# Kernel optimization log

Hardware: AMD Instinct MI355X
Metric: run time of the kernel (lower is better)

Reference implementation:

```python
import jax, jax.numpy as jnp
import numpy as np

N, D, G, H, M = 500000, 128, 64, 128, 256  # bag size, local_dim, global_dim, attn_hidden, mlp_hidden
TEMP = 1.0


def setup_inputs() -> dict:
    key = jax.random.key(0)
    ks = jax.random.split(key, 8)
    s = 0.05
    return {
        "bag": jax.random.normal(ks[0], (N, D), jnp.float32),
        "global_feat": jax.random.normal(ks[1], (G,), jnp.float32),
        # attention_V: Linear(D, H) + Tanh
        "Wv": jax.random.normal(ks[2], (H, D), jnp.float32) * s,
        "bv": jnp.zeros((H,), jnp.float32),
        # attention_U: Linear(D, H) + Sigmoid
        "Wu": jax.random.normal(ks[3], (H, D), jnp.float32) * s,
        "bu": jnp.zeros((H,), jnp.float32),
        # attention_weights: Linear(H, 1)
        "Ww": jax.random.normal(ks[4], (1, H), jnp.float32) * s,
        "bw": jnp.zeros((1,), jnp.float32),
        "W1": jax.random.normal(ks[5], (M, D + G), jnp.float32) * s,
        "b1": jnp.zeros((M,), jnp.float32),
        "W2": jax.random.normal(ks[6], (1, M), jnp.float32) * s,
        "b2": jnp.zeros((1,), jnp.float32),
    }


def reference(bag, global_feat, Wv, bv, Wu, bu, Ww, bw, W1, b1, W2, b2):
    # feature_extractor = Identity (use_feature_extractor=False); dropout = identity (eval)
    V = jnp.tanh(bag @ Wv.T + bv)            # [N, H]
    U = jax.nn.sigmoid(bag @ Wu.T + bu)      # [N, H]
    Ggate = V * U                            # [N, H]
    A_raw = Ggate @ Ww.T + bw                # [N, 1]
    alpha = jax.nn.softmax(A_raw / TEMP, axis=0)  # softmax over bag dim
    bag_embedding = alpha.T @ bag            # [1, D]
    fused = jnp.concatenate([bag_embedding, global_feat.reshape(1, -1)], axis=1)  # [1, D+G]
    h = jax.nn.leaky_relu(fused @ W1.T + b1, negative_slope=0.01)  # [1, M]
    score = h @ W2.T + b2                    # [1, 1]
    return (score, alpha)
```

## Files before the change

### kernel.cpp

```cpp
#include <hip/hip_runtime.h>
#include <hip/hip_bf16.h>

#define N_BAG 500000
#define DIM   128
#define ROWS_PER_ITER 32
#define ITERS 21
#define ROWS_PER_BLOCK 672
#define NBLK  768
#define GDIM  64
#define LDB   136

typedef __attribute__((ext_vector_type(8))) __bf16 bf16x8;
typedef __attribute__((ext_vector_type(4))) __bf16 bf16x4;
typedef __attribute__((ext_vector_type(4))) float  f32x4;

union BF8 { bf16x8 v; __bf16 e[8]; };

__device__ __forceinline__ float fast_rcp(float x) { return __builtin_amdgcn_rcpf(x); }

__global__ __launch_bounds__(256, 3)
void attn_pass1(const float* __restrict__ bag,
                const float* __restrict__ Wv, const float* __restrict__ bv,
                const float* __restrict__ Wu, const float* __restrict__ bu,
                const float* __restrict__ Ww, const float* __restrict__ bw,
                float* __restrict__ aOut,
                float* __restrict__ blkS, float* __restrict__ blkW,
                float* __restrict__ Eacc, float* __restrict__ Ssum)
{
    __shared__ __align__(16) unsigned char smem[2 * ROWS_PER_ITER * LDB * 2];
    __shared__ __align__(16) float a_part[ROWS_PER_ITER][4];

    typedef __bf16 XsRow[ROWS_PER_ITER][LDB];
    XsRow* Xs = (XsRow*)smem;
    float (*fin)[4] = (float(*)[4])smem;

    const int tid = threadIdx.x;
    const int w   = tid >> 6;
    const int L   = tid & 63;
    const int m16 = L & 15;
    const int q   = L >> 4;
    const int hh  = L >> 5;
    const int c32 = L & 31;
    const int blk = blockIdx.x;
    const int rowBase = blk * ROWS_PER_BLOCK;

    if (blk == 0) {
        if (tid < DIM) Eacc[tid] = 0.0f;
        if (tid == DIM) Ssum[0] = 0.0f;
    }

    BF8 fv[2][4], fu[2][4];
    float bvv[2], buu[2], www[2];
#pragma unroll
    for (int ht = 0; ht < 2; ++ht) {
        const int h = w*32 + ht*16 + m16;
        bvv[ht] = bv[h]; buu[ht] = bu[h]; www[ht] = Ww[h];
#pragma unroll
        for (int s = 0; s < 4; ++s) {
            const int d0 = s*32 + q*8;
            const float4 v0 = *(const float4*)(Wv + h*DIM + d0);
            const float4 v1 = *(const float4*)(Wv + h*DIM + d0 + 4);
            const float4 u0 = *(const float4*)(Wu + h*DIM + d0);
            const float4 u1 = *(const float4*)(Wu + h*DIM + d0 + 4);
            fv[ht][s].e[0]=(__bf16)v0.x; fv[ht][s].e[1]=(__bf16)v0.y;
            fv[ht][s].e[2]=(__bf16)v0.z; fv[ht][s].e[3]=(__bf16)v0.w;
            fv[ht][s].e[4]=(__bf16)v1.x; fv[ht][s].e[5]=(__bf16)v1.y;
            fv[ht][s].e[6]=(__bf16)v1.z; fv[ht][s].e[7]=(__bf16)v1.w;
            fu[ht][s].e[0]=(__bf16)u0.x; fu[ht][s].e[1]=(__bf16)u0.y;
            fu[ht][s].e[2]=(__bf16)u0.z; fu[ht][s].e[3]=(__bf16)u0.w;
            fu[ht][s].e[4]=(__bf16)u1.x; fu[ht][s].e[5]=(__bf16)u1.y;
            fu[ht][s].e[6]=(__bf16)u1.z; fu[ht][s].e[7]=(__bf16)u1.w;
        }
    }
    const float bw0 = bw[0];

    float4 stg[4];
#pragma unroll
    for (int i = 0; i < 4; ++i) {
        int r = rowBase + i*8 + w*2 + hh;
        if (r >= N_BAG) r = N_BAG - 1;
        stg[i] = *(const float4*)(bag + (size_t)r*DIM + c32*4);
    }

    float s_acc = 0.0f;
    float wacc0 = 0.f, wacc1 = 0.f, wacc2 = 0.f, wacc3 = 0.f;

    for (int it = 0; it < ITERS; ++it) {
        const int buf = it & 1;
        const int tileStart = rowBase + it*ROWS_PER_ITER;

#pragma unroll
        for (int i = 0; i < 4; ++i) {
            const int row = i*8 + w*2 + hh;
            bf16x4 pk;
            pk.x = (__bf16)stg[i].x; pk.y = (__bf16)stg[i].y;
            pk.z = (__bf16)stg[i].z; pk.w = (__bf16)stg[i].w;
            *(bf16x4*)&Xs[buf][row][c32*4] = pk;
        }
        __syncthreads();

        if (it + 1 < ITERS) {
            const int ts2 = tileStart + ROWS_PER_ITER;
#pragma unroll
            for (int i = 0; i < 4; ++i) {
                int r = ts2 + i*8 + w*2 + hh;
                if (r >= N_BAG) r = N_BAG - 1;
                stg[i] = *(const float4*)(bag + (size_t)r*DIM + c32*4);
            }
        }

#pragma unroll
        for (int r = 0; r < 2; ++r) {
            f32x4 accV[2], accU[2];
#pragma unroll
            for (int ht = 0; ht < 2; ++ht) {
                accV[ht] = (f32x4){0.f,0.f,0.f,0.f};
                accU[ht] = (f32x4){0.f,0.f,0.f,0.f};
            }
#pragma unroll
            for (int s = 0; s < 4; ++s) {
                const bf16x8 af = *(const bf16x8*)&Xs[buf][r*16 + m16][s*32 + q*8];
#pragma unroll
                for (int ht = 0; ht < 2; ++ht) {
                    accV[ht] = __builtin_amdgcn_mfma_f32_16x16x32_bf16(af, fv[ht][s].v, accV[ht], 0, 0, 0);
                    accU[ht] = __builtin_amdgcn_mfma_f32_16x16x32_bf16(af, fu[ht][s].v, accU[ht], 0, 0, 0);
                }
            }
            float psum[4];
#pragma unroll
            for (int g = 0; g < 4; ++g) {
                float p = 0.0f;
#pragma unroll
                for (int ht = 0; ht < 2; ++ht) {
                    const float z = accV[ht][g] + bvv[ht];
                    const float y = accU[ht][g] + buu[ht];
                    const float A = __expf(2.0f*z);
                    const float B = __expf(y);
                    p += (A - 1.0f) * B * www[ht] * fast_rcp((A + 1.0f) * (B + 1.0f));
                }
                p += __shfl_xor(p, 1); p += __shfl_xor(p, 2);
                p += __shfl_xor(p, 4); p += __shfl_xor(p, 8);
                psum[g] = p;
            }
            if (m16 == 0) {
#pragma unroll
                for (int g = 0; g < 4; ++g)
                    a_part[r*16 + q*4 + g][w] = psum[g];
            }
        }
        __syncthreads();

        const int li = L & 31;
        const float4 ap = *(const float4*)&a_part[li][0];
        float a = ap.x + ap.y + ap.z + ap.w + bw0;
        const int grow = tileStart + li;
        if (w == 0 && L < 32 && grow < N_BAG) aOut[grow] = a;
        if (grow >= N_BAG) a = -1e30f;
        const float e = __expf(a);
        if (w == 0 && L < 32) s_acc += e;

        float s0 = 0.f, s1 = 0.f, s2 = 0.f, s3 = 0.f;
#pragma unroll
        for (int i = 0; i < 4; ++i) {
            const int row = i*8 + w*2 + hh;
            const float ei = __shfl(e, row);
            const bf16x4 xb = *(const bf16x4*)&Xs[buf][row][c32*4];
            s0 += ei * (float)xb.x; s1 += ei * (float)xb.y;
            s2 += ei * (float)xb.z; s3 += ei * (float)xb.w;
        }
        wacc0 += s0; wacc1 += s1; wacc2 += s2; wacc3 += s3;
    }

    float st = s_acc;
    st += __shfl_xor(st, 1);  st += __shfl_xor(st, 2);
    st += __shfl_xor(st, 4);  st += __shfl_xor(st, 8);
    st += __shfl_xor(st, 16); st += __shfl_xor(st, 32);

    __syncthreads();
    fin[tid][0] = wacc0; fin[tid][1] = wacc1;
    fin[tid][2] = wacc2; fin[tid][3] = wacc3;
    if (L == 0) a_part[0][w] = st;
    __syncthreads();
    if (tid < 128) {
        float v = 0.0f;
#pragma unroll
        for (int k = 0; k < 8; ++k) {
            const int t = (k >> 1)*64 + (k & 1)*32 + (tid >> 2);
            v += fin[t][tid & 3];
        }
        blkW[blk*DIM + tid] = v;
    }
    if (tid == 0) blkS[blk] = a_part[0][0];

    (void)Eacc; (void)Ssum;
}

__global__ void headA(const float* __restrict__ blkW, const float* __restrict__ blkS,
                      float* __restrict__ E, float* __restrict__ Ssum)
{
    const int tid = threadIdx.x;
    const int c = tid & 127, g = tid >> 7;
    const int b0 = blockIdx.x * 16;
    float acc = 0.0f;
#pragma unroll
    for (int t = 0; t < 8; ++t) {
        const int b = b0 + g*8 + t;
        acc += blkW[b*DIM + c];
    }
    atomicAdd(&E[c], acc);

    if (tid < 16) {
        float sv = blkS[b0 + tid];
        sv += __shfl_xor(sv, 1); sv += __shfl_xor(sv, 2);
        sv += __shfl_xor(sv, 4); sv += __shfl_xor(sv, 8);
        if (tid == 0) atomicAdd(Ssum, sv);
    }
}

__global__ void headB(const float* __restrict__ E, const float* __restrict__ Ssum,
                      const float* __restrict__ gfeat,
                      const float* __restrict__ W1, const float* __restrict__ b1,
                      const float* __restrict__ W2, const float* __restrict__ b2,
                      float* __restrict__ out)
{
    __shared__ float f[DIM + GDIM];
    __shared__ float red[256];
    const int tid = threadIdx.x;

    const float invS = 1.0f / Ssum[0];
    if (tid < DIM)             f[tid] = E[tid] * invS;
    else if (tid < DIM + GDIM) f[tid] = gfeat[tid - DIM];
    __syncthreads();

    float a2 = b1[tid];
    const float4* w1p = (const float4*)(W1 + tid * (DIM + GDIM));
    const float4* fp  = (const float4*)f;
#pragma unroll 4
    for (int k = 0; k < (DIM + GDIM) / 4; ++k) {
        const float4 a4 = w1p[k]; const float4 f4 = fp[k];
        a2 += a4.x*f4.x + a4.y*f4.y + a4.z*f4.z + a4.w*f4.w;
    }
    const float h = a2 > 0.0f ? a2 : 0.01f * a2;
    red[tid] = h * W2[tid]; __syncthreads();
    for (int s = 128; s > 0; s >>= 1) {
        if (tid < s) red[tid] += red[tid + s];
        __syncthreads();
    }
    if (tid == 0) out[0] = red[0] + b2[0];
}

__global__ void alpha_kernel(float* __restrict__ alpha, const float* __restrict__ Ssum)
{
    const int i = blockIdx.x * blockDim.x + threadIdx.x;
    const float invS = 1.0f / Ssum[0];
    if (i * 4 < N_BAG) {
        float4 a4 = *(float4*)(alpha + i*4);
        a4.x = __expf(a4.x) * invS; a4.y = __expf(a4.y) * invS;
        a4.z = __expf(a4.z) * invS; a4.w = __expf(a4.w) * invS;
        *(float4*)(alpha + i*4) = a4;
    }
}

extern "C" void kernel_launch(void* const* d_in, const int* in_sizes, int n_in,
                              void* d_out, int out_size, void* d_ws, size_t ws_size,
                              hipStream_t stream)
{
    const float* bag   = (const float*)d_in[0];
    const float* gfeat = (const float*)d_in[1];
    const float* Wv    = (const float*)d_in[2];
    const float* bv    = (const float*)d_in[3];
    const float* Wu    = (const float*)d_in[4];
    const float* bu    = (const float*)d_in[5];
    const float* Ww    = (const float*)d_in[6];
    const float* bw    = (const float*)d_in[7];
    const float* W1    = (const float*)d_in[8];
    const float* b1    = (const float*)d_in[9];
    const float* W2    = (const float*)d_in[10];
    const float* b2    = (const float*)d_in[11];
    float* out = (float*)d_out;
    float* ws  = (float*)d_ws;

    float* blkS = ws;
    float* blkW = ws + 1024;
    float* Eacc = ws + 1024 + 98304;
    float* Ssum = ws + 1024 + 98304 + 128;

    attn_pass1<<<NBLK, 256, 0, stream>>>(bag, Wv, bv, Wu, bu, Ww, bw,
                                         out + 1, blkS, blkW, Eacc, Ssum);
    headA<<<48, 256, 0, stream>>>(blkW, blkS, Eacc, Ssum);
    headB<<<1, 256, 0, stream>>>(Eacc, Ssum, gfeat, W1, b1, W2, b2, out);
    alpha_kernel<<<(N_BAG/4 + 255) / 256, 256, 0, stream>>>(out + 1, Ssum);
}
```

Before: 399.8 us.

## Register double-buffer bag tiles, single LDS buffer, fuse head into alpha kernel

The attention pass now keeps two register staging sets and alternates between them in an unrolled pair loop, so only one LDS tile buffer is needed. The softmax-weighted accumulation reads the fp32 staged registers instead of re-reading bf16 values from LDS, and the biases are folded into the MFMA accumulator initialization. The single-block MLP head is merged into the alpha-normalization kernel, removing one kernel launch. The aim is to cut LDS traffic and launch overhead, at the cost of higher register pressure from holding two staging sets.

```diff
diff --git a/kernel.cpp b/kernel.cpp
--- a/kernel.cpp
+++ b/kernel.cpp
@@ -27,11 +27,11 @@
                 float* __restrict__ blkS, float* __restrict__ blkW,
                 float* __restrict__ Eacc, float* __restrict__ Ssum)
 {
-    __shared__ __align__(16) unsigned char smem[2 * ROWS_PER_ITER * LDB * 2];
+    __shared__ __align__(16) unsigned char smem[ROWS_PER_ITER * LDB * 2];
     __shared__ __align__(16) float a_part[ROWS_PER_ITER][4];
 
-    typedef __bf16 XsRow[ROWS_PER_ITER][LDB];
-    XsRow* Xs = (XsRow*)smem;
+    typedef __bf16 XsT[LDB];
+    XsT* Xs = (XsT*)smem;
     float (*fin)[4] = (float(*)[4])smem;
 
     const int tid = threadIdx.x;
@@ -74,102 +74,98 @@
     }
     const float bw0 = bw[0];
 
-    float4 stg[4];
-#pragma unroll
-    for (int i = 0; i < 4; ++i) {
-        int r = rowBase + i*8 + w*2 + hh;
-        if (r >= N_BAG) r = N_BAG - 1;
-        stg[i] = *(const float4*)(bag + (size_t)r*DIM + c32*4);
-    }
-
     float s_acc = 0.0f;
     float wacc0 = 0.f, wacc1 = 0.f, wacc2 = 0.f, wacc3 = 0.f;
-
-    for (int it = 0; it < ITERS; ++it) {
-        const int buf = it & 1;
-        const int tileStart = rowBase + it*ROWS_PER_ITER;
-
-#pragma unroll
-        for (int i = 0; i < 4; ++i) {
-            const int row = i*8 + w*2 + hh;
-            bf16x4 pk;
-            pk.x = (__bf16)stg[i].x; pk.y = (__bf16)stg[i].y;
-            pk.z = (__bf16)stg[i].z; pk.w = (__bf16)stg[i].w;
-            *(bf16x4*)&Xs[buf][row][c32*4] = pk;
-        }
-        __syncthreads();
-
-        if (it + 1 < ITERS) {
-            const int ts2 = tileStart + ROWS_PER_ITER;
-#pragma unroll
-            for (int i = 0; i < 4; ++i) {
-                int r = ts2 + i*8 + w*2 + hh;
-                if (r >= N_BAG) r = N_BAG - 1;
-                stg[i] = *(const float4*)(bag + (size_t)r*DIM + c32*4);
-            }
-        }
-
-#pragma unroll
-        for (int r = 0; r < 2; ++r) {
-            f32x4 accV[2], accU[2];
-#pragma unroll
-            for (int ht = 0; ht < 2; ++ht) {
-                accV[ht] = (f32x4){0.f,0.f,0.f,0.f};
-                accU[ht] = (f32x4){0.f,0.f,0.f,0.f};
-            }
-#pragma unroll
-            for (int s = 0; s < 4; ++s) {
-                const bf16x8 af = *(const bf16x8*)&Xs[buf][r*16 + m16][s*32 + q*8];
-#pragma unroll
-                for (int ht = 0; ht < 2; ++ht) {
-                    accV[ht] = __builtin_amdgcn_mfma_f32_16x16x32_bf16(af, fv[ht][s].v, accV[ht], 0, 0, 0);
-                    accU[ht] = __builtin_amdgcn_mfma_f32_16x16x32_bf16(af, fu[ht][s].v, accU[ht], 0, 0, 0);
-                }
-            }
-            float psum[4];
-#pragma unroll
-            for (int g = 0; g < 4; ++g) {
-                float p = 0.0f;
-#pragma unroll
-                for (int ht = 0; ht < 2; ++ht) {
-                    const float z = accV[ht][g] + bvv[ht];
-                    const float y = accU[ht][g] + buu[ht];
-                    const float A = __expf(2.0f*z);
-                    const float B = __expf(y);
-                    p += (A - 1.0f) * B * www[ht] * fast_rcp((A + 1.0f) * (B + 1.0f));
-                }
-                p += __shfl_xor(p, 1); p += __shfl_xor(p, 2);
-                p += __shfl_xor(p, 4); p += __shfl_xor(p, 8);
-                psum[g] = p;
-            }
-            if (m16 == 0) {
-#pragma unroll
-                for (int g = 0; g < 4; ++g)
-                    a_part[r*16 + q*4 + g][w] = psum[g];
-            }
-        }
-        __syncthreads();
-
-        const int li = L & 31;
-        const float4 ap = *(const float4*)&a_part[li][0];
-        float a = ap.x + ap.y + ap.z + ap.w + bw0;
-        const int grow = tileStart + li;
-        if (w == 0 && L < 32 && grow < N_BAG) aOut[grow] = a;
-        if (grow >= N_BAG) a = -1e30f;
-        const float e = __expf(a);
-        if (w == 0 && L < 32) s_acc += e;
-
-        float s0 = 0.f, s1 = 0.f, s2 = 0.f, s3 = 0.f;
-#pragma unroll
-        for (int i = 0; i < 4; ++i) {
-            const int row = i*8 + w*2 + hh;
-            const float ei = __shfl(e, row);
-            const bf16x4 xb = *(const bf16x4*)&Xs[buf][row][c32*4];
-            s0 += ei * (float)xb.x; s1 += ei * (float)xb.y;
-            s2 += ei * (float)xb.z; s3 += ei * (float)xb.w;
-        }
-        wacc0 += s0; wacc1 += s1; wacc2 += s2; wacc3 += s3;
-    }
+    float4 stgA[4], stgB[4];
+
+#define LOADT(DST, T) do {                                                    \
+    const int ts_ = rowBase + (T)*ROWS_PER_ITER;                              \
+    _Pragma("unroll")                                                         \
+    for (int i_ = 0; i_ < 4; ++i_) {                                          \
+        int r_ = ts_ + i_*8 + w*2 + hh;                                       \
+        if (r_ >= N_BAG) r_ = N_BAG - 1;                                      \
+        DST[i_] = *(const float4*)(bag + (size_t)r_*DIM + c32*4);             \
+    } } while (0)
+
+#define STEP(T, CUR, NXT, DO_PF) do {                                         \
+    _Pragma("unroll")                                                         \
+    for (int i_ = 0; i_ < 4; ++i_) {                                          \
+        const int row_ = i_*8 + w*2 + hh;                                     \
+        bf16x4 pk_;                                                           \
+        pk_.x = (__bf16)CUR[i_].x; pk_.y = (__bf16)CUR[i_].y;                 \
+        pk_.z = (__bf16)CUR[i_].z; pk_.w = (__bf16)CUR[i_].w;                 \
+        *(bf16x4*)&Xs[row_][c32*4] = pk_;                                     \
+    }                                                                         \
+    __syncthreads();                 \
+    if (DO_PF) LOADT(NXT, (T) + 1);                                           \
+    _Pragma("unroll")                                                         \
+    for (int r_ = 0; r_ < 2; ++r_) {                                          \
+        f32x4 accV_[2], accU_[2];                                             \
+        _Pragma("unroll")                                                     \
+        for (int ht_ = 0; ht_ < 2; ++ht_) {                                   \
+            accV_[ht_] = (f32x4){bvv[ht_], bvv[ht_], bvv[ht_], bvv[ht_]};     \
+            accU_[ht_] = (f32x4){buu[ht_], buu[ht_], buu[ht_], buu[ht_]};     \
+        }                                                                     \
+        _Pragma("unroll")                                                     \
+        for (int s_ = 0; s_ < 4; ++s_) {                                      \
+            const bf16x8 af_ = *(const bf16x8*)&Xs[r_*16 + m16][s_*32 + q*8]; \
+            _Pragma("unroll")                                                 \
+            for (int ht_ = 0; ht_ < 2; ++ht_) {                               \
+                accV_[ht_] = __builtin_amdgcn_mfma_f32_16x16x32_bf16(af_, fv[ht_][s_].v, accV_[ht_], 0, 0, 0); \
+                accU_[ht_] = __builtin_amdgcn_mfma_f32_16x16x32_bf16(af_, fu[ht_][s_].v, accU_[ht_], 0, 0, 0); \
+            }                                                                 \
+        }                                                                     \
+        \
+        float psum_[4];                                                       \
+        _Pragma("unroll")                                                     \
+        for (int g_ = 0; g_ < 4; ++g_) {                                      \
+            float p_ = 0.0f;                                                  \
+            _Pragma("unroll")                                                 \
+            for (int ht_ = 0; ht_ < 2; ++ht_) {                               \
+                const float z_ = accV_[ht_][g_];       \
+                const float y_ = accU_[ht_][g_];                              \
+                const float A_ = __expf(2.0f*z_);                             \
+                const float B_ = __expf(y_);                                  \
+                p_ += (A_ - 1.0f) * B_ * www[ht_] * fast_rcp((A_ + 1.0f) * (B_ + 1.0f)); \
+            }                                                                 \
+            p_ += __shfl_xor(p_, 1); p_ += __shfl_xor(p_, 2);                 \
+            p_ += __shfl_xor(p_, 4); p_ += __shfl_xor(p_, 8);                 \
+            psum_[g_] = p_;                                                   \
+        }                                                                     \
+        if (m16 == 0) {                                                       \
+            _Pragma("unroll")                                                 \
+            for (int g_ = 0; g_ < 4; ++g_)                                    \
+                a_part[r_*16 + q*4 + g_][w] = psum_[g_];                      \
+        }                                                                     \
+    }                                                                         \
+    __syncthreads();              \
+    {                                                                         \
+        const int li_ = L & 31;                                               \
+        const float4 ap_ = *(const float4*)&a_part[li_][0];                   \
+        float a_ = ap_.x + ap_.y + ap_.z + ap_.w + bw0;                       \
+        const int grow_ = rowBase + (T)*ROWS_PER_ITER + li_;                  \
+        if (w == 0 && L < 32 && grow_ < N_BAG) aOut[grow_] = a_;              \
+        if (grow_ >= N_BAG) a_ = -1e30f;    \
+        const float e_ = __expf(a_);                                          \
+        if (w == 0 && L < 32) s_acc += e_;         \
+        _Pragma("unroll")                                                     \
+        for (int i_ = 0; i_ < 4; ++i_) {                                      \
+            const int row_ = i_*8 + w*2 + hh;                                 \
+            const float ei_ = __shfl(e_, row_);                               \
+            wacc0 += ei_ * CUR[i_].x; wacc1 += ei_ * CUR[i_].y;               \
+            wacc2 += ei_ * CUR[i_].z; wacc3 += ei_ * CUR[i_].w;               \
+        }                                                                     \
+    } } while (0)
+
+    LOADT(stgA, 0);
+    for (int itp = 0; itp < (ITERS - 1) / 2; ++itp) {
+        STEP(2*itp,     stgA, stgB, 1);
+        STEP(2*itp + 1, stgB, stgA, 1);
+    }
+    STEP(ITERS - 1, stgA, stgB, 0);
+
+#undef STEP
+#undef LOADT
 
     float st = s_acc;
     st += __shfl_xor(st, 1);  st += __shfl_xor(st, 2);
@@ -217,47 +213,44 @@
     }
 }
 
-__global__ void headB(const float* __restrict__ E, const float* __restrict__ Ssum,
-                      const float* __restrict__ gfeat,
-                      const float* __restrict__ W1, const float* __restrict__ b1,
-                      const float* __restrict__ W2, const float* __restrict__ b2,
-                      float* __restrict__ out)
-{
-    __shared__ float f[DIM + GDIM];
-    __shared__ float red[256];
+__global__ void alpha_head(float* __restrict__ alpha, const float* __restrict__ Ssum,
+                           const float* __restrict__ E, const float* __restrict__ gfeat,
+                           const float* __restrict__ W1, const float* __restrict__ b1,
+                           const float* __restrict__ W2, const float* __restrict__ b2,
+                           float* __restrict__ out)
+{
     const int tid = threadIdx.x;
-
-    const float invS = 1.0f / Ssum[0];
-    if (tid < DIM)             f[tid] = E[tid] * invS;
-    else if (tid < DIM + GDIM) f[tid] = gfeat[tid - DIM];
-    __syncthreads();
-
-    float a2 = b1[tid];
-    const float4* w1p = (const float4*)(W1 + tid * (DIM + GDIM));
-    const float4* fp  = (const float4*)f;
-#pragma unroll 4
-    for (int k = 0; k < (DIM + GDIM) / 4; ++k) {
-        const float4 a4 = w1p[k]; const float4 f4 = fp[k];
-        a2 += a4.x*f4.x + a4.y*f4.y + a4.z*f4.z + a4.w*f4.w;
-    }
-    const float h = a2 > 0.0f ? a2 : 0.01f * a2;
-    red[tid] = h * W2[tid]; __syncthreads();
-    for (int s = 128; s > 0; s >>= 1) {
-        if (tid < s) red[tid] += red[tid + s];
-        __syncthreads();
-    }
-    if (tid == 0) out[0] = red[0] + b2[0];
-}
-
-__global__ void alpha_kernel(float* __restrict__ alpha, const float* __restrict__ Ssum)
-{
-    const int i = blockIdx.x * blockDim.x + threadIdx.x;
+    const int i = blockIdx.x * blockDim.x + tid;
     const float invS = 1.0f / Ssum[0];
     if (i * 4 < N_BAG) {
         float4 a4 = *(float4*)(alpha + i*4);
         a4.x = __expf(a4.x) * invS; a4.y = __expf(a4.y) * invS;
         a4.z = __expf(a4.z) * invS; a4.w = __expf(a4.w) * invS;
         *(float4*)(alpha + i*4) = a4;
+    }
+
+    if (blockIdx.x == 0) {
+        __shared__ __align__(16) float f[DIM + GDIM];
+        __shared__ float red[256];
+        if (tid < DIM)             f[tid] = E[tid] * invS;
+        else if (tid < DIM + GDIM) f[tid] = gfeat[tid - DIM];
+        __syncthreads();
+
+        float a2 = b1[tid];
+        const float4* w1p = (const float4*)(W1 + tid * (DIM + GDIM));
+        const float4* fp  = (const float4*)f;
+#pragma unroll 4
+        for (int k = 0; k < (DIM + GDIM) / 4; ++k) {
+            const float4 a4 = w1p[k]; const float4 f4 = fp[k];
+            a2 += a4.x*f4.x + a4.y*f4.y + a4.z*f4.z + a4.w*f4.w;
+        }
+        const float h = a2 > 0.0f ? a2 : 0.01f * a2;
+        red[tid] = h * W2[tid]; __syncthreads();
+        for (int s = 128; s > 0; s >>= 1) {
+            if (tid < s) red[tid] += red[tid + s];
+            __syncthreads();
+        }
+        if (tid == 0) out[0] = red[0] + b2[0];
     }
 }
 
@@ -288,6 +281,6 @@
     attn_pass1<<<NBLK, 256, 0, stream>>>(bag, Wv, bv, Wu, bu, Ww, bw,
                                          out + 1, blkS, blkW, Eacc, Ssum);
     headA<<<48, 256, 0, stream>>>(blkW, blkS, Eacc, Ssum);
-    headB<<<1, 256, 0, stream>>>(Eacc, Ssum, gfeat, W1, b1, W2, b2, out);
-    alpha_kernel<<<(N_BAG/4 + 255) / 256, 256, 0, stream>>>(out + 1, Ssum);
-}
+    alpha_head<<<(N_BAG/4 + 255) / 256, 256, 0, stream>>>(out + 1, Ssum, Eacc,
+                                                          gfeat, W1, b1, W2, b2, out);
+}
```

New measurement: 423.1 us. +5.8%, slower.
